# Performance work log

Hardware: AMD Instinct MI355X
Metric: run time of the kernel (lower is better)

Reference implementation:

```python
import jax, jax.numpy as jnp
import numpy as np

NUM_ITERATIONS = 100
EPS = 1e-6
LIPSCHITZ_COEFF = 0.9


def _l2_normalize(x, axis=None, eps=1e-12):
    return x * jax.lax.rsqrt((x * x).sum(axis=axis, keepdims=True) + eps)


def setup_inputs() -> dict:
    key = jax.random.key(0)
    k1, k2, k3, k4 = jax.random.split(key, 4)
    B, D_in, D_out = 32768, 1024, 1024
    x = jax.random.normal(k1, (B, D_in), dtype=jnp.float32)
    # TruncatedNormal(stddev=1/sqrt(fan_in)) approximated by scaled normal
    w = jax.random.normal(k2, (D_in, D_out), dtype=jnp.float32) / np.sqrt(D_in)
    b = jax.random.normal(k3, (D_out,), dtype=jnp.float32)
    u0 = jax.random.normal(k4, (1, D_out), dtype=jnp.float32)
    return {"x": x, "w": w, "b": b, "u0": u0}


def reference(x, w, b, u0):
    d_in = w.shape[0]

    # 100-step power iteration: tight sequential dependency chain of GEMV pairs.
    def body(i, carry):
        u, _ = carry
        v = _l2_normalize(jnp.matmul(u, w.T), eps=EPS)   # [1, d_in]
        u = _l2_normalize(jnp.matmul(v, w), eps=EPS)     # [1, d_out]
        return (u, v)

    v_init = jnp.zeros((1, d_in), dtype=w.dtype)
    u, v = jax.lax.fori_loop(0, NUM_ITERATIONS, body, (u0, v_init))
    u = jax.lax.stop_gradient(u)
    v = jax.lax.stop_gradient(v)

    sigma = jnp.matmul(jnp.matmul(v, w), u.T)[0, 0]      # spectral norm estimate
    factor = jnp.maximum(1.0, sigma / LIPSCHITZ_COEFF)
    w_norm = w / factor

    out = jnp.dot(x, w_norm) + b
    return out
```

## Files before the change

kernel.cpp:

```cpp
#include <hip/hip_runtime.h>
#include <hip/hip_bf16.h>
#include <cstdint>
#include <cstddef>

#define DDIM 1024
#define BROWS 32768

typedef __attribute__((ext_vector_type(8))) short short8;
typedef __attribute__((ext_vector_type(4))) float floatx4;

__device__ __forceinline__ float bf2f(unsigned short u) {
  return __uint_as_float(((unsigned int)u) << 16);
}
__device__ __forceinline__ unsigned short f2bf(float f) {
  unsigned int u = __float_as_uint(f);
  u += 0x7FFFu + ((u >> 16) & 1u);
  return (unsigned short)(u >> 16);
}

__device__ __forceinline__ void load_lds16(const void* g, void* l) {
  __builtin_amdgcn_global_load_lds(
      (const __attribute__((address_space(1))) unsigned int*)g,
      (__attribute__((address_space(3))) unsigned int*)l,
      16, 0, 0);
}

__global__ void __launch_bounds__(256, 2)
big_gemm(const float* __restrict__ Af, const unsigned short* __restrict__ Bt,
         float* __restrict__ Outf, const float* __restrict__ inv_ptr,
         const float* __restrict__ bias)
{
  __shared__ __align__(16) char smem[16896];
  unsigned short* As = (unsigned short*)smem;
  unsigned short* Bs = (unsigned short*)(smem + 8192);
  float* epi = (float*)smem;

  const int tid  = threadIdx.x;
  const int lane = tid & 63;
  const int wid  = tid >> 6;
  const int wr = wid >> 1, wc = wid & 1;
  const int g = lane >> 4, r = lane & 15;

  const int bm0 = (int)(blockIdx.x & 255) * 128;
  const int bn0 = (int)(blockIdx.x >> 8) * 128;

  const floatx4 zero4 = {0.f, 0.f, 0.f, 0.f};
  floatx4 acc[4][4];
#pragma unroll
  for (int m = 0; m < 4; ++m)
#pragma unroll
    for (int n = 0; n < 4; ++n) acc[m][n] = zero4;

  for (int kk = 0; kk < DDIM; kk += 32) {
    __syncthreads();
#pragma unroll
    for (int p = 0; p < 2; ++p) {
      const int o = p * 4096 + tid * 16;
      const int row = o >> 6;
      const int cole = (o & 63) >> 1;
      load_lds16(Bt + (size_t)(bn0 + row) * DDIM + kk + cole, (char*)Bs + o);
    }
#pragma unroll
    for (int p = 0; p < 2; ++p) {
      const int o = p * 4096 + tid * 16;
      const int row = o >> 6;
      const int cole = (o & 63) >> 1;
      const float4* s = (const float4*)(Af + (size_t)(bm0 + row) * DDIM + kk + cole);
      float4 x0 = s[0], x1 = s[1];
      short8 t;
      t[0] = (short)f2bf(x0.x); t[1] = (short)f2bf(x0.y);
      t[2] = (short)f2bf(x0.z); t[3] = (short)f2bf(x0.w);
      t[4] = (short)f2bf(x1.x); t[5] = (short)f2bf(x1.y);
      t[6] = (short)f2bf(x1.z); t[7] = (short)f2bf(x1.w);
      *(short8*)((char*)As + o) = t;
    }
    __syncthreads();

    short8 afr[4], bfr[4];
#pragma unroll
    for (int m = 0; m < 4; ++m)
      afr[m] = *(const short8*)((const char*)As + (wr * 64 + m * 16 + r) * 64 + g * 16);
#pragma unroll
    for (int n = 0; n < 4; ++n)
      bfr[n] = *(const short8*)((const char*)Bs + (wc * 64 + n * 16 + r) * 64 + g * 16);
#pragma unroll
    for (int m = 0; m < 4; ++m)
#pragma unroll
      for (int n = 0; n < 4; ++n)
        acc[m][n] = __builtin_amdgcn_mfma_f32_16x16x32_bf16(afr[m], bfr[n], acc[m][n], 0, 0, 0);
  }

  const float inv = *inv_ptr;
  float bv[4];
#pragma unroll
  for (int n = 0; n < 4; ++n) bv[n] = bias[bn0 + wc * 64 + n * 16 + r];

#pragma unroll
  for (int m = 0; m < 4; ++m) {
    __syncthreads();
#pragma unroll
    for (int n = 0; n < 4; ++n)
#pragma unroll
      for (int q = 0; q < 4; ++q)
        epi[(wr * 16 + g * 4 + q) * 132 + wc * 64 + n * 16 + r] =
            acc[m][n][q] * inv + bv[n];
    __syncthreads();
    const int lrow = tid >> 3;
    const int lc0  = (tid & 7) * 16;
    const int grow = bm0 + m * 16 + (lrow & 15) + (lrow >> 4) * 64;
    float4* dst = (float4*)(Outf + (size_t)grow * DDIM + bn0 + lc0);
    const float4* sv = (const float4*)(epi + lrow * 132 + lc0);
    dst[0] = sv[0]; dst[1] = sv[1]; dst[2] = sv[2]; dst[3] = sv[3];
  }
}

__global__ void __launch_bounds__(256, 2)
sq_gemm(const unsigned short* __restrict__ A, const unsigned short* __restrict__ Bt,
        unsigned short* __restrict__ Out, const float* __restrict__ in_max,
        float* __restrict__ out_max)
{
  __shared__ __align__(16) unsigned short As[2][4096];
  __shared__ __align__(16) unsigned short Bs[2][4096];
  __shared__ float redw[4];

  const int tid  = threadIdx.x;
  const int lane = tid & 63;
  const int wid  = tid >> 6;
  const int wr = wid >> 1, wc = wid & 1;
  const int g = lane >> 4, r = lane & 15;

  const int bm0 = (int)(blockIdx.x >> 4) * 64;
  const int bn0 = (int)(blockIdx.x & 15) * 64;

  const int so    = tid * 16;
  const int srow0 = so >> 7;
  const int sc16  = (so >> 4) & 7;
  const int scs   = sc16 ^ (srow0 & 7);
  const unsigned short* aSrc0 = A  + (size_t)(bm0 + srow0) * DDIM + scs * 8;
  const unsigned short* aSrc1 = A  + (size_t)(bm0 + 32 + srow0) * DDIM + scs * 8;
  const unsigned short* bSrc0 = Bt + (size_t)(bn0 + srow0) * DDIM + scs * 8;
  const unsigned short* bSrc1 = Bt + (size_t)(bn0 + 32 + srow0) * DDIM + scs * 8;

  const floatx4 zero4 = {0.f, 0.f, 0.f, 0.f};
  floatx4 acc[2][2];
#pragma unroll
  for (int fm = 0; fm < 2; ++fm)
#pragma unroll
    for (int fn = 0; fn < 2; ++fn) acc[fm][fn] = zero4;

  load_lds16(aSrc0, (char*)&As[0][0] + so);
  load_lds16(aSrc1, (char*)&As[0][0] + 4096 + so);
  load_lds16(bSrc0, (char*)&Bs[0][0] + so);
  load_lds16(bSrc1, (char*)&Bs[0][0] + 4096 + so);
  __syncthreads();

  int buf = 0;
  for (int t = 0; t < 16; ++t) {
    if (t + 1 < 16) {
      const int kk = (t + 1) * 64;
      load_lds16(aSrc0 + kk, (char*)&As[buf ^ 1][0] + so);
      load_lds16(aSrc1 + kk, (char*)&As[buf ^ 1][0] + 4096 + so);
      load_lds16(bSrc0 + kk, (char*)&Bs[buf ^ 1][0] + so);
      load_lds16(bSrc1 + kk, (char*)&Bs[buf ^ 1][0] + 4096 + so);
    }
#pragma unroll
    for (int ks = 0; ks < 2; ++ks) {
      const int chunk = ((ks << 2) + g) ^ (r & 7);
      short8 af[2], bf[2];
#pragma unroll
      for (int fm = 0; fm < 2; ++fm) {
        const int arow = wr * 32 + fm * 16 + r;
        af[fm] = *(const short8*)((const char*)&As[buf][0] + (arow << 7) + (chunk << 4));
      }
#pragma unroll
      for (int fn = 0; fn < 2; ++fn) {
        const int brow = wc * 32 + fn * 16 + r;
        bf[fn] = *(const short8*)((const char*)&Bs[buf][0] + (brow << 7) + (chunk << 4));
      }
#pragma unroll
      for (int fm = 0; fm < 2; ++fm)
#pragma unroll
        for (int fn = 0; fn < 2; ++fn)
          acc[fm][fn] = __builtin_amdgcn_mfma_f32_16x16x32_bf16(af[fm], bf[fn], acc[fm][fn], 0, 0, 0);
    }
    __syncthreads();
    buf ^= 1;
  }

  float c = 1.0f;
  if (in_max != nullptr) {
    int e;
    (void)frexpf(*in_max, &e);
    c = ldexpf(1.0f, -e);
  }
  const float c2 = c * c;
  float lmax = 0.0f;
#pragma unroll
  for (int fm = 0; fm < 2; ++fm) {
#pragma unroll
    for (int fn = 0; fn < 2; ++fn) {
      const int ocol = bn0 + wc * 32 + fn * 16 + r;
#pragma unroll
      for (int q = 0; q < 4; ++q) {
        const int orow = bm0 + wr * 32 + fm * 16 + g * 4 + q;
        float v = acc[fm][fn][q] * c2;
        Out[(size_t)orow * DDIM + ocol] = f2bf(v);
        lmax = fmaxf(lmax, fabsf(v));
      }
    }
  }
#pragma unroll
  for (int off = 32; off > 0; off >>= 1) lmax = fmaxf(lmax, __shfl_down(lmax, off));
  if (lane == 0) redw[wid] = lmax;
  __syncthreads();
  if (tid == 0) {
    float m = fmaxf(fmaxf(redw[0], redw[1]), fmaxf(redw[2], redw[3]));
    atomicMax((unsigned int*)out_max, __float_as_uint(m));
  }
}

__global__ void __launch_bounds__(256)
transpose_bf16(const float* __restrict__ W, unsigned short* __restrict__ WT)
{
  __shared__ float tile[64][65];
  const int bx = blockIdx.x & 15;
  const int by = blockIdx.x >> 4;
  const int tid = threadIdx.x;
  const int c = tid & 63;
  const int r0 = tid >> 6;
#pragma unroll
  for (int p = 0; p < 16; ++p) {
    int kr = p * 4 + r0;
    tile[kr][c] = W[(size_t)(bx * 64 + kr) * DDIM + by * 64 + c];
  }
  __syncthreads();
#pragma unroll
  for (int p = 0; p < 16; ++p) {
    int nr = p * 4 + r0;
    WT[(size_t)(by * 64 + nr) * DDIM + bx * 64 + c] = f2bf(tile[c][nr]);
  }
}

__global__ void __launch_bounds__(256)
gemv_pow(const unsigned short* __restrict__ P, const float* __restrict__ vin,
         float* __restrict__ vout)
{
  const int tid = threadIdx.x;
  const int lane = tid & 63;
  const int wid = tid >> 6;
  float vs[16];
  const float4* vv = (const float4*)(vin + lane * 16);
#pragma unroll
  for (int i = 0; i < 4; ++i) {
    float4 t = vv[i];
    vs[i * 4 + 0] = t.x; vs[i * 4 + 1] = t.y; vs[i * 4 + 2] = t.z; vs[i * 4 + 3] = t.w;
  }
#pragma unroll
  for (int rr = 0; rr < 4; ++rr) {
    const int row = (int)blockIdx.x * 16 + wid * 4 + rr;
    const unsigned short* pr = P + (size_t)row * DDIM + lane * 16;
    short8 p0 = *(const short8*)pr;
    short8 p1 = *(const short8*)(pr + 8);
    float s = 0.f;
#pragma unroll
    for (int e = 0; e < 8; ++e) s += bf2f((unsigned short)p0[e]) * vs[e];
#pragma unroll
    for (int e = 0; e < 8; ++e) s += bf2f((unsigned short)p1[e]) * vs[8 + e];
#pragma unroll
    for (int off = 32; off > 0; off >>= 1) s += __shfl_down(s, off);
    if (lane == 0) vout[row] = s * 0x1p-12f;
  }
}

__global__ void __launch_bounds__(256)
v_kernel(const float* __restrict__ W, const float* __restrict__ d,
         float* __restrict__ v_un, float* __restrict__ vpart)
{
  __shared__ float wsum[4];
  const int tid = threadIdx.x;
  const int lane = tid & 63;
  const int wid = tid >> 6;
  float vs[16];
  const float4* dv = (const float4*)(d + lane * 16);
#pragma unroll
  for (int i = 0; i < 4; ++i) {
    float4 t = dv[i];
    vs[i * 4 + 0] = t.x; vs[i * 4 + 1] = t.y; vs[i * 4 + 2] = t.z; vs[i * 4 + 3] = t.w;
  }
  float ssq = 0.f;
#pragma unroll
  for (int rr = 0; rr < 4; ++rr) {
    const int row = (int)blockIdx.x * 16 + wid * 4 + rr;
    const float4* wrow = (const float4*)(W + (size_t)row * DDIM + lane * 16);
    float s = 0.f;
#pragma unroll
    for (int i = 0; i < 4; ++i) {
      float4 t = wrow[i];
      s += t.x * vs[i * 4 + 0] + t.y * vs[i * 4 + 1] + t.z * vs[i * 4 + 2] + t.w * vs[i * 4 + 3];
    }
#pragma unroll
    for (int off = 32; off > 0; off >>= 1) s += __shfl_down(s, off);
    if (lane == 0) { v_un[row] = s; ssq += s * s; }
  }
  if (lane == 0) wsum[wid] = ssq;
  __syncthreads();
  if (tid == 0) vpart[blockIdx.x] = (wsum[0] + wsum[1]) + (wsum[2] + wsum[3]);
}

__global__ void __launch_bounds__(256)
t_fin_kernel(const float* __restrict__ W, const float* __restrict__ v_un,
             float* __restrict__ vpart, float* __restrict__ tpart,
             unsigned int* __restrict__ counter, float* __restrict__ inv_out)
{
  __shared__ float part[8][33];
  __shared__ unsigned int sticket;
  const int tid = threadIdx.x;
  const int col = (int)blockIdx.x * 32 + (tid & 31);
  const int ch = tid >> 5;
  float s = 0.f;
  const int i0 = ch * 128;
  for (int i = i0; i < i0 + 128; ++i)
    s += v_un[i] * W[(size_t)i * DDIM + col];
  part[ch][tid & 31] = s;
  __syncthreads();
  if (tid < 32) {
    float t = 0.f;
#pragma unroll
    for (int c2 = 0; c2 < 8; ++c2) t += part[c2][tid];
    part[0][tid] = t * t;
  }
  __syncthreads();
  if (tid == 0) {
    float ss = 0.f;
#pragma unroll
    for (int c = 0; c < 32; ++c) ss += part[0][c];
    tpart[blockIdx.x] = ss;
    __threadfence();
    sticket = atomicAdd(counter, 1u);
  }
  __syncthreads();
  if (sticket == 31) {
    __threadfence();
    float val = 0.f;
    if (tid < 64)
      val = __uint_as_float(atomicOr((unsigned int*)&vpart[tid], 0u));
    part[tid >> 5][tid & 31] = val;
    __syncthreads();
    if (tid == 0) {
      float sv = 0.f;
      for (int i = 0; i < 64; ++i) sv += part[i >> 5][i & 31];
      float stq = 0.f;
      for (int i = 0; i < 32; ++i)
        stq += __uint_as_float(atomicOr((unsigned int*)&tpart[i], 0u));
      float sigma = sqrtf(stq / sv);
      inv_out[0] = (sigma > 0.9f) ? (0.9f / sigma) : 1.0f;
    }
  }
}

extern "C" void kernel_launch(void* const* d_in, const int* in_sizes, int n_in,
                              void* d_out, int out_size, void* d_ws, size_t ws_size,
                              hipStream_t stream)
{
  const float* x  = (const float*)d_in[0];
  const float* w  = (const float*)d_in[1];
  const float* b  = (const float*)d_in[2];
  const float* u0 = (const float*)d_in[3];
  float* out = (float*)d_out;

  char* ws = (char*)d_ws;
  float* scal = (float*)ws;
  float* u_a  = (float*)(ws + 0x1000);
  float* u_b  = (float*)(ws + 0x2000);
  float* v_un = (float*)(ws + 0x3000);
  unsigned short* WT = (unsigned short*)(ws + 0x4000);
  unsigned short* P0 = (unsigned short*)(ws + 0x204000);
  unsigned short* P1 = (unsigned short*)(ws + 0x404000);

  hipMemsetAsync(d_ws, 0, 4096, stream);
  hipLaunchKernelGGL(transpose_bf16, dim3(256), dim3(256), 0, stream, w, WT);

  hipLaunchKernelGGL(sq_gemm, dim3(256), dim3(256), 0, stream,
                     WT, WT, P0, (const float*)nullptr, &scal[0]);
  hipLaunchKernelGGL(sq_gemm, dim3(256), dim3(256), 0, stream,
                     P0, P0, P1, &scal[0], &scal[1]);
  hipLaunchKernelGGL(sq_gemm, dim3(256), dim3(256), 0, stream,
                     P1, P1, P0, &scal[1], &scal[2]);
  hipLaunchKernelGGL(sq_gemm, dim3(256), dim3(256), 0, stream,
                     P0, P0, P1, &scal[2], &scal[3]);
  hipLaunchKernelGGL(sq_gemm, dim3(256), dim3(256), 0, stream,
                     P1, P1, P0, &scal[3], &scal[4]);
  hipLaunchKernelGGL(sq_gemm, dim3(256), dim3(256), 0, stream,
                     P0, P0, P1, &scal[4], &scal[5]);

  hipLaunchKernelGGL(gemv_pow, dim3(64), dim3(256), 0, stream, P1, u0, u_a);
  hipLaunchKernelGGL(gemv_pow, dim3(64), dim3(256), 0, stream, P1, u_a, u_b);
  hipLaunchKernelGGL(gemv_pow, dim3(64), dim3(256), 0, stream, P1, u_b, u_a);

  hipLaunchKernelGGL(v_kernel, dim3(64), dim3(256), 0, stream, w, u_a, v_un, &scal[16]);
  hipLaunchKernelGGL(t_fin_kernel, dim3(32), dim3(256), 0, stream,
                     w, v_un, &scal[16], &scal[80],
                     (unsigned int*)&scal[120], &scal[8]);

  hipLaunchKernelGGL(big_gemm, dim3(2048), dim3(256), 0, stream,
                     x, WT, out, &scal[8], b);
}
```

Baseline: 262.2 us.

## Double-buffer LDS tiles in big GEMM to overlap loads with MFMA

Replaces the single-buffered K loop with a two-stage LDS ping-pong. The next A tile (fp32 to bf16) is loaded into registers and the next B tile is issued via global_load_lds before the MFMAs on the current tile. The A conversion and store happen after compute, so each iteration needs one barrier instead of two. This hides global latency behind compute, but doubles shared memory to about 33 KB and raises register pressure, which may reduce occupancy.

```diff
diff --git a/kernel.cpp b/kernel.cpp
--- a/kernel.cpp
+++ b/kernel.cpp
@@ -30,9 +30,7 @@
          float* __restrict__ Outf, const float* __restrict__ inv_ptr,
          const float* __restrict__ bias)
 {
-  __shared__ __align__(16) char smem[16896];
-  unsigned short* As = (unsigned short*)smem;
-  unsigned short* Bs = (unsigned short*)(smem + 8192);
+  __shared__ __align__(16) char smem[33280];
   float* epi = (float*)smem;
 
   const int tid  = threadIdx.x;
@@ -44,6 +42,13 @@
   const int bm0 = (int)(blockIdx.x & 255) * 128;
   const int bn0 = (int)(blockIdx.x >> 8) * 128;
 
+  const int strow = tid >> 2;
+  const int stcol = (tid & 3) * 8;
+  const float* aB0 = Af + (size_t)(bm0 + strow) * DDIM + stcol;
+  const float* aB1 = Af + (size_t)(bm0 + 64 + strow) * DDIM + stcol;
+  const unsigned short* bB0 = Bt + (size_t)(bn0 + strow) * DDIM + stcol;
+  const unsigned short* bB1 = Bt + (size_t)(bn0 + 64 + strow) * DDIM + stcol;
+
   const floatx4 zero4 = {0.f, 0.f, 0.f, 0.f};
   floatx4 acc[4][4];
 #pragma unroll
@@ -51,43 +56,73 @@
 #pragma unroll
     for (int n = 0; n < 4; ++n) acc[m][n] = zero4;
 
-  for (int kk = 0; kk < DDIM; kk += 32) {
-    __syncthreads();
-#pragma unroll
-    for (int p = 0; p < 2; ++p) {
-      const int o = p * 4096 + tid * 16;
-      const int row = o >> 6;
-      const int cole = (o & 63) >> 1;
-      load_lds16(Bt + (size_t)(bn0 + row) * DDIM + kk + cole, (char*)Bs + o);
-    }
-#pragma unroll
-    for (int p = 0; p < 2; ++p) {
-      const int o = p * 4096 + tid * 16;
-      const int row = o >> 6;
-      const int cole = (o & 63) >> 1;
-      const float4* s = (const float4*)(Af + (size_t)(bm0 + row) * DDIM + kk + cole);
-      float4 x0 = s[0], x1 = s[1];
-      short8 t;
-      t[0] = (short)f2bf(x0.x); t[1] = (short)f2bf(x0.y);
-      t[2] = (short)f2bf(x0.z); t[3] = (short)f2bf(x0.w);
-      t[4] = (short)f2bf(x1.x); t[5] = (short)f2bf(x1.y);
-      t[6] = (short)f2bf(x1.z); t[7] = (short)f2bf(x1.w);
-      *(short8*)((char*)As + o) = t;
-    }
-    __syncthreads();
+  {
+    load_lds16(bB0, smem + 16384 + tid * 16);
+    load_lds16(bB1, smem + 16384 + 4096 + tid * 16);
+    float4 n0 = *(const float4*)aB0;
+    float4 n1 = *(const float4*)(aB0 + 4);
+    float4 n2 = *(const float4*)aB1;
+    float4 n3 = *(const float4*)(aB1 + 4);
+    short8 t0, t1;
+    t0[0] = (short)f2bf(n0.x); t0[1] = (short)f2bf(n0.y);
+    t0[2] = (short)f2bf(n0.z); t0[3] = (short)f2bf(n0.w);
+    t0[4] = (short)f2bf(n1.x); t0[5] = (short)f2bf(n1.y);
+    t0[6] = (short)f2bf(n1.z); t0[7] = (short)f2bf(n1.w);
+    t1[0] = (short)f2bf(n2.x); t1[1] = (short)f2bf(n2.y);
+    t1[2] = (short)f2bf(n2.z); t1[3] = (short)f2bf(n2.w);
+    t1[4] = (short)f2bf(n3.x); t1[5] = (short)f2bf(n3.y);
+    t1[6] = (short)f2bf(n3.z); t1[7] = (short)f2bf(n3.w);
+    *(short8*)(smem + tid * 16) = t0;
+    *(short8*)(smem + 4096 + tid * 16) = t1;
+  }
+  __syncthreads();
+
+  for (int t = 0; t < 32; ++t) {
+    const int co = (t & 1) << 13;
+    char* curA = smem + co;
+    char* curB = smem + 16384 + co;
+    char* nxtA = smem + (co ^ 8192);
+    char* nxtB = smem + 16384 + (co ^ 8192);
+
+    float4 n0, n1, n2, n3;
+    const bool pref = (t < 31);
+    if (pref) {
+      const int ko = (t + 1) * 32;
+      n0 = *(const float4*)(aB0 + ko);
+      n1 = *(const float4*)(aB0 + ko + 4);
+      n2 = *(const float4*)(aB1 + ko);
+      n3 = *(const float4*)(aB1 + ko + 4);
+      load_lds16(bB0 + ko, nxtB + tid * 16);
+      load_lds16(bB1 + ko, nxtB + 4096 + tid * 16);
+    }
 
     short8 afr[4], bfr[4];
 #pragma unroll
     for (int m = 0; m < 4; ++m)
-      afr[m] = *(const short8*)((const char*)As + (wr * 64 + m * 16 + r) * 64 + g * 16);
+      afr[m] = *(const short8*)(curA + (wr * 64 + m * 16 + r) * 64 + g * 16);
 #pragma unroll
     for (int n = 0; n < 4; ++n)
-      bfr[n] = *(const short8*)((const char*)Bs + (wc * 64 + n * 16 + r) * 64 + g * 16);
+      bfr[n] = *(const short8*)(curB + (wc * 64 + n * 16 + r) * 64 + g * 16);
 #pragma unroll
     for (int m = 0; m < 4; ++m)
 #pragma unroll
       for (int n = 0; n < 4; ++n)
         acc[m][n] = __builtin_amdgcn_mfma_f32_16x16x32_bf16(afr[m], bfr[n], acc[m][n], 0, 0, 0);
+
+    if (pref) {
+      short8 t0, t1;
+      t0[0] = (short)f2bf(n0.x); t0[1] = (short)f2bf(n0.y);
+      t0[2] = (short)f2bf(n0.z); t0[3] = (short)f2bf(n0.w);
+      t0[4] = (short)f2bf(n1.x); t0[5] = (short)f2bf(n1.y);
+      t0[6] = (short)f2bf(n1.z); t0[7] = (short)f2bf(n1.w);
+      t1[0] = (short)f2bf(n2.x); t1[1] = (short)f2bf(n2.y);
+      t1[2] = (short)f2bf(n2.z); t1[3] = (short)f2bf(n2.w);
+      t1[4] = (short)f2bf(n3.x); t1[5] = (short)f2bf(n3.y);
+      t1[6] = (short)f2bf(n3.z); t1[7] = (short)f2bf(n3.w);
+      *(short8*)(nxtA + tid * 16) = t0;
+      *(short8*)(nxtA + 4096 + tid * 16) = t1;
+    }
+    __syncthreads();
   }
 
   const float inv = *inv_ptr;
```

New measurement: 278.0 us. +6.0%, slower.
